# Kernel optimization log

Measured on AMD Instinct MI355X. Metric: run time of the kernel, lower is better.

Reference implementation:

```python
import jax, jax.numpy as jnp
import numpy as np

B, S, DIM, H, HD, K, DEPTH = 2, 2048, 1024, 16, 64, 64, 8
SCALE = 1.0 / np.sqrt(HD)


def _build_cantor_routes(seq_len: int, k: int, depth: int) -> np.ndarray:
    # Vectorized version of CantorAttention._build_cantor_routes
    pos = np.arange(seq_len, dtype=np.float64)
    x = pos / max(1, seq_len - 1)
    x = np.clip(x, 1e-06, 1.0 - 1e-06)
    cantor = np.zeros(seq_len, dtype=np.float64)
    factor = 0.5
    for _ in range(depth):
        x = x * 3.0
        digit = np.floor(x)
        x = x - digit
        cantor += factor * (digit == 2.0)
        factor *= 0.5
    cantor = cantor.astype(np.float32)
    # k nearest positions in Cantor space for each position
    dist = np.abs(cantor[:, None] - cantor[None, :])  # [S, S]
    routes = np.argsort(dist, axis=1, kind='stable')[:, :k]  # [S, k]
    return routes.astype(np.int32)


def setup_inputs() -> dict:
    key = jax.random.key(0)
    k1, k2, k3, k4, k5 = jax.random.split(key, 5)
    s = 1.0 / np.sqrt(DIM)
    return {
        'x': jax.random.normal(k1, (B, S, DIM), dtype=jnp.float32),
        'w_qkv': jax.random.normal(k2, (3 * DIM, DIM), dtype=jnp.float32) * s,
        'b_qkv': jax.random.normal(k3, (3 * DIM,), dtype=jnp.float32) * 0.01,
        'w_out': jax.random.normal(k4, (DIM, DIM), dtype=jnp.float32) * s,
        'b_out': jax.random.normal(k5, (DIM,), dtype=jnp.float32) * 0.01,
        'routes': jnp.asarray(_build_cantor_routes(S, K, DEPTH)),
    }


def reference(x, w_qkv, b_qkv, w_out, b_out, routes):
    b, s, _ = x.shape
    # QKV projection (torch Linear: y = x @ W.T + b)
    qkv = x @ w_qkv.T + b_qkv                       # [B, S, 3*DIM]
    qkv = qkv.reshape(b, s, 3, H, HD).transpose(2, 0, 3, 1, 4)  # [3, B, H, S, HD]
    q, k, v = qkv[0], qkv[1], qkv[2]                # each [B, H, S, HD]
    # Gather k/v at Cantor neighbor routes: [B, H, S, K, HD]
    k_g = jnp.take(k, routes, axis=2)
    v_g = jnp.take(v, routes, axis=2)
    scores = jnp.einsum('bhqd,bhqkd->bhqk', q, k_g) * SCALE
    attn = jax.nn.softmax(scores, axis=-1)
    out = jnp.einsum('bhqk,bhqkd->bhqd', attn, v_g)  # [B, H, S, HD]
    out = out.transpose(0, 2, 1, 3).reshape(b, s, DIM)
    return out @ w_out.T + b_out
```

## Files before the change

kernel.cpp:

```cpp
#include <hip/hip_runtime.h>

#define BQ   2
#define SQ   2048
#define DIMQ 1024
#define HQ   16
#define HDQ  64
#define KQ   64
#define QKV_STRIDE (3 * DIMQ)

typedef __attribute__((ext_vector_type(8))) short short8;
typedef __attribute__((ext_vector_type(4))) float floatx4;

typedef const __attribute__((address_space(1))) unsigned short* gas_t;
typedef __attribute__((address_space(3))) unsigned short* las_t;

__device__ __forceinline__ unsigned short f2b(float f) {
    union { float f; unsigned int u; } x; x.f = f;
    unsigned int r = x.u + 0x7fffu + ((x.u >> 16) & 1u);
    return (unsigned short)(r >> 16);
}
__device__ __forceinline__ float b2f(unsigned short u) {
    union { unsigned int u; float f; } x; x.u = ((unsigned int)u) << 16;
    return x.f;
}

__global__ __launch_bounds__(256) void cast3_f32_bf16(const float* __restrict__ s0, unsigned short* __restrict__ d0, int n0,
                                                      const float* __restrict__ s1, unsigned short* __restrict__ d1, int n1,
                                                      const float* __restrict__ s2, unsigned short* __restrict__ d2, int n2) {
    int i = blockIdx.x * blockDim.x + threadIdx.x;
    const float* s; unsigned short* d;
    if (i < n0)                { s = s0; d = d0; }
    else if (i < n0 + n1)      { s = s1; d = d1; i -= n0; }
    else if (i < n0 + n1 + n2) { s = s2; d = d2; i -= n0 + n1; }
    else return;
    float4 v = ((const float4*)s)[i];
    ushort4 o;
    o.x = f2b(v.x); o.y = f2b(v.y); o.z = f2b(v.z); o.w = f2b(v.w);
    ((ushort4*)d)[i] = o;
}

template <int BM, int BN, typename CT>
__global__ __launch_bounds__(256) void gemm_bf16_nt(const unsigned short* __restrict__ A,
                                                    const unsigned short* __restrict__ B,
                                                    const float* __restrict__ bias,
                                                    CT* __restrict__ C,
                                                    int M, int N, int K) {
    constexpr int MI = BM / 32;
    constexpr int NJ = BN / 32;
    __shared__ unsigned short As[BM * 64];
    __shared__ unsigned short Bs[BN * 64];

    const int tid  = threadIdx.x;
    const int lane = tid & 63;
    const int wv   = tid >> 6;
    const int wm   = (wv >> 1) * (BM / 2);
    const int wn   = (wv & 1) * (BN / 2);
    const int fr   = lane & 15;
    const int fq   = lane >> 4;

    const int m0 = blockIdx.y * BM;
    const int n0 = blockIdx.x * BN;

    floatx4 acc[MI][NJ];
#pragma unroll
    for (int i = 0; i < MI; ++i)
#pragma unroll
        for (int j = 0; j < NJ; ++j) acc[i][j] = (floatx4)(0.f);

    const unsigned short* Ab = A + (size_t)m0 * K;
    const unsigned short* Bb = B + (size_t)n0 * K;

    for (int k0 = 0; k0 < K; k0 += 64) {
#pragma unroll
        for (int c = 0; c < (BM + BN) * 8; c += 256) {
            const int cc = c + tid;
            if (cc < BM * 8) {
                const int row = cc >> 3;
                const int kc  = ((cc & 7) ^ (row & 7)) << 3;
                __builtin_amdgcn_global_load_lds(
                    (gas_t)(Ab + (size_t)row * K + k0 + kc),
                    (las_t)&As[cc * 8], 16, 0, 0);
            } else {
                const int c2  = cc - BM * 8;
                const int row = c2 >> 3;
                const int kc  = ((c2 & 7) ^ (row & 7)) << 3;
                __builtin_amdgcn_global_load_lds(
                    (gas_t)(Bb + (size_t)row * K + k0 + kc),
                    (las_t)&Bs[c2 * 8], 16, 0, 0);
            }
        }
        __syncthreads();

#pragma unroll
        for (int ks = 0; ks < 2; ++ks) {
            short8 af[MI], bf[NJ];
#pragma unroll
            for (int i = 0; i < MI; ++i) {
                const int row = wm + i * 16 + fr;
                const int pos = (ks * 4 + fq) ^ (row & 7);
                af[i] = *(const short8*)&As[row * 64 + pos * 8];
            }
#pragma unroll
            for (int j = 0; j < NJ; ++j) {
                const int row = wn + j * 16 + fr;
                const int pos = (ks * 4 + fq) ^ (row & 7);
                bf[j] = *(const short8*)&Bs[row * 64 + pos * 8];
            }
#pragma unroll
            for (int i = 0; i < MI; ++i)
#pragma unroll
                for (int j = 0; j < NJ; ++j)
                    acc[i][j] = __builtin_amdgcn_mfma_f32_16x16x32_bf16(af[i], bf[j], acc[i][j], 0, 0, 0);
        }
        __syncthreads();
    }

    float bv[NJ];
#pragma unroll
    for (int j = 0; j < NJ; ++j) bv[j] = bias[n0 + wn + j * 16 + fr];
#pragma unroll
    for (int i = 0; i < MI; ++i) {
#pragma unroll
        for (int r = 0; r < 4; ++r) {
            const size_t row = (size_t)(m0 + wm + i * 16 + fq * 4 + r);
#pragma unroll
            for (int j = 0; j < NJ; ++j) {
                const float v = acc[i][j][r] + bv[j];
                if constexpr (sizeof(CT) == 2)
                    C[row * N + n0 + wn + j * 16 + fr] = (CT)f2b(v);
                else
                    C[row * N + n0 + wn + j * 16 + fr] = (CT)v;
            }
        }
    }
}

__global__ __launch_bounds__(256) void attn_kernel(const unsigned short* __restrict__ qkv,
                                                   const int* __restrict__ routes,
                                                   unsigned short* __restrict__ out) {
    __shared__ int   r_s[KQ];
    __shared__ float m_s[128], l_s[128];
    __shared__ float o_part[8][128];

    const int t  = threadIdx.x;
    const int id = blockIdx.x;
    const int bq = (id & 7) * 512 + (id >> 3);
    const int b  = bq >> 11;
    const int q  = bq & 2047;

    if (t < KQ) r_s[t] = routes[q * KQ + t];

    const int g  = t >> 7;
    const int th = t & 127;
    const int h  = th >> 3;
    const int d0 = (t & 7) * 8;

    float qf[8];
    {
        const short8 q8 = *(const short8*)&qkv[((size_t)bq * 3) * DIMQ + h * HDQ + d0];
#pragma unroll
        for (int e = 0; e < 8; ++e) qf[e] = b2f((unsigned short)q8[e]);
    }
    __syncthreads();

    const unsigned short* baseK = qkv + ((size_t)b * SQ * 3 + 1) * DIMQ + h * HDQ + d0;
    const unsigned short* baseV = qkv + ((size_t)b * SQ * 3 + 2) * DIMQ + h * HDQ + d0;

    float m = -1e30f, l = 0.f;
    float o[8];
#pragma unroll
    for (int e = 0; e < 8; ++e) o[e] = 0.f;

    short8 kb[2], vb[2];
#pragma unroll
    for (int i = 0; i < 2; ++i) {
        const size_t roff = (size_t)r_s[i * 2 + g] * QKV_STRIDE;
        kb[i] = *(const short8*)(baseK + roff);
        vb[i] = *(const short8*)(baseV + roff);
    }

#pragma unroll 8
    for (int jj = 0; jj < KQ / 2; ++jj) {
        const int slot = jj & 1;
        const short8 k8 = kb[slot];
        const short8 v8 = vb[slot];
        if (jj + 2 < KQ / 2) {
            const size_t roff = (size_t)r_s[(jj + 2) * 2 + g] * QKV_STRIDE;
            kb[slot] = *(const short8*)(baseK + roff);
            vb[slot] = *(const short8*)(baseV + roff);
        }
        float p = 0.f;
#pragma unroll
        for (int e = 0; e < 8; ++e) p += qf[e] * b2f((unsigned short)k8[e]);
        p += __shfl_xor(p, 1, 64);
        p += __shfl_xor(p, 2, 64);
        p += __shfl_xor(p, 4, 64);
        const float s  = p * 0.125f;
        const float mn = fmaxf(m, s);
        const float al = __expf(m - mn);
        const float pe = __expf(s - mn);
        l = l * al + pe;
#pragma unroll
        for (int e = 0; e < 8; ++e) o[e] = o[e] * al + pe * b2f((unsigned short)v8[e]);
        m = mn;
    }

    if (g == 1) {
        m_s[th] = m; l_s[th] = l;
#pragma unroll
        for (int e = 0; e < 8; ++e) o_part[e][th] = o[e];
    }
    __syncthreads();
    if (g == 0) {
        const float m1 = m_s[th], l1 = l_s[th];
        const float mm = fmaxf(m, m1);
        const float a0 = __expf(m - mm);
        const float a1 = __expf(m1 - mm);
        const float inv = 1.0f / (l * a0 + l1 * a1);
        float oo[8];
#pragma unroll
        for (int e = 0; e < 8; ++e) oo[e] = (o[e] * a0 + o_part[e][th] * a1) * inv;
        ushort4 lo, hi;
        lo.x = f2b(oo[0]); lo.y = f2b(oo[1]); lo.z = f2b(oo[2]); lo.w = f2b(oo[3]);
        hi.x = f2b(oo[4]); hi.y = f2b(oo[5]); hi.z = f2b(oo[6]); hi.w = f2b(oo[7]);
        ushort4* dst = (ushort4*)&out[(size_t)bq * DIMQ + h * HDQ + d0];
        dst[0] = lo; dst[1] = hi;
    }
}

extern "C" void kernel_launch(void* const* d_in, const int* in_sizes, int n_in,
                              void* d_out, int out_size, void* d_ws, size_t ws_size,
                              hipStream_t stream) {
    const float* x      = (const float*)d_in[0];
    const float* w_qkv  = (const float*)d_in[1];
    const float* b_qkv  = (const float*)d_in[2];
    const float* w_out  = (const float*)d_in[3];
    const float* b_out  = (const float*)d_in[4];
    const int*   routes = (const int*)d_in[5];
    float* out = (float*)d_out;

    char* ws = (char*)d_ws;
    unsigned short* qkvb  = (unsigned short*)ws;
    unsigned short* xb    = (unsigned short*)(ws + 25165824);
    unsigned short* attnb = xb;
    unsigned short* wqb   = (unsigned short*)(ws + 33554432);
    unsigned short* wob   = (unsigned short*)(ws + 39845888);

    const int M = BQ * SQ;
    dim3 blk(256);

    {
        const int n0 = M * DIMQ / 4, n1 = 3 * DIMQ * DIMQ / 4, n2 = DIMQ * DIMQ / 4;
        cast3_f32_bf16<<<(n0 + n1 + n2 + 255) / 256, blk, 0, stream>>>(
            x, xb, n0, w_qkv, wqb, n1, w_out, wob, n2);
    }

    gemm_bf16_nt<128, 128, unsigned short><<<dim3(3 * DIMQ / 128, M / 128), blk, 0, stream>>>(
        xb, wqb, b_qkv, qkvb, M, 3 * DIMQ, DIMQ);

    attn_kernel<<<BQ * SQ, blk, 0, stream>>>(qkvb, routes, attnb);

    gemm_bf16_nt<128, 64, float><<<dim3(DIMQ / 64, M / 128), blk, 0, stream>>>(
        attnb, wob, b_out, out, M, DIMQ, DIMQ);
}
```

Measured before the change: 188.0 us.

## Replace online softmax with two-pass exact softmax and base-2 exponent

The gathered attention kernel now computes all 32 scores per thread first, takes one max, exponentiates with exp2f using a query pre-scaled by scale*log2(e), and then accumulates V in a separate loop. This drops the per-step rescaling of the running output and the two exponentials per key that the online softmax needed. The K and V prefetch depth grows from two to four gathered rows. In exchange it holds 32 score registers plus deeper prefetch buffers, which raises register pressure and may lower occupancy, and V loads no longer overlap with the K loop.

```diff
diff --git a/kernel.cpp b/kernel.cpp
--- a/kernel.cpp
+++ b/kernel.cpp
@@ -159,35 +159,27 @@
     {
         const short8 q8 = *(const short8*)&qkv[((size_t)bq * 3) * DIMQ + h * HDQ + d0];
 #pragma unroll
-        for (int e = 0; e < 8; ++e) qf[e] = b2f((unsigned short)q8[e]);
+        for (int e = 0; e < 8; ++e) qf[e] = b2f((unsigned short)q8[e]) * 0.18033688011112042f;
     }
     __syncthreads();
 
     const unsigned short* baseK = qkv + ((size_t)b * SQ * 3 + 1) * DIMQ + h * HDQ + d0;
     const unsigned short* baseV = qkv + ((size_t)b * SQ * 3 + 2) * DIMQ + h * HDQ + d0;
 
-    float m = -1e30f, l = 0.f;
-    float o[8];
-#pragma unroll
-    for (int e = 0; e < 8; ++e) o[e] = 0.f;
-
-    short8 kb[2], vb[2];
-#pragma unroll
-    for (int i = 0; i < 2; ++i) {
+    float s[32];
+    short8 kb[4];
+#pragma unroll
+    for (int i = 0; i < 4; ++i) {
         const size_t roff = (size_t)r_s[i * 2 + g] * QKV_STRIDE;
         kb[i] = *(const short8*)(baseK + roff);
-        vb[i] = *(const short8*)(baseV + roff);
-    }
-
-#pragma unroll 8
-    for (int jj = 0; jj < KQ / 2; ++jj) {
-        const int slot = jj & 1;
+    }
+#pragma unroll
+    for (int jj = 0; jj < 32; ++jj) {
+        const int slot = jj & 3;
         const short8 k8 = kb[slot];
-        const short8 v8 = vb[slot];
-        if (jj + 2 < KQ / 2) {
-            const size_t roff = (size_t)r_s[(jj + 2) * 2 + g] * QKV_STRIDE;
+        if (jj + 4 < 32) {
+            const size_t roff = (size_t)r_s[(jj + 4) * 2 + g] * QKV_STRIDE;
             kb[slot] = *(const short8*)(baseK + roff);
-            vb[slot] = *(const short8*)(baseV + roff);
         }
         float p = 0.f;
 #pragma unroll
@@ -195,14 +187,49 @@
         p += __shfl_xor(p, 1, 64);
         p += __shfl_xor(p, 2, 64);
         p += __shfl_xor(p, 4, 64);
-        const float s  = p * 0.125f;
-        const float mn = fmaxf(m, s);
-        const float al = __expf(m - mn);
-        const float pe = __expf(s - mn);
-        l = l * al + pe;
-#pragma unroll
-        for (int e = 0; e < 8; ++e) o[e] = o[e] * al + pe * b2f((unsigned short)v8[e]);
-        m = mn;
+        s[jj] = p;
+    }
+
+    short8 vb[4];
+#pragma unroll
+    for (int i = 0; i < 4; ++i) {
+        const size_t roff = (size_t)r_s[i * 2 + g] * QKV_STRIDE;
+        vb[i] = *(const short8*)(baseV + roff);
+    }
+
+    float mx[16];
+#pragma unroll
+    for (int i = 0; i < 16; ++i) mx[i] = fmaxf(s[i], s[i + 16]);
+#pragma unroll
+    for (int i = 0; i < 8; ++i) mx[i] = fmaxf(mx[i], mx[i + 8]);
+#pragma unroll
+    for (int i = 0; i < 4; ++i) mx[i] = fmaxf(mx[i], mx[i + 4]);
+    const float m = fmaxf(fmaxf(mx[0], mx[1]), fmaxf(mx[2], mx[3]));
+
+    float l0 = 0.f, l1 = 0.f, l2 = 0.f, l3 = 0.f;
+#pragma unroll
+    for (int jj = 0; jj < 32; jj += 4) {
+        s[jj + 0] = exp2f(s[jj + 0] - m); l0 += s[jj + 0];
+        s[jj + 1] = exp2f(s[jj + 1] - m); l1 += s[jj + 1];
+        s[jj + 2] = exp2f(s[jj + 2] - m); l2 += s[jj + 2];
+        s[jj + 3] = exp2f(s[jj + 3] - m); l3 += s[jj + 3];
+    }
+    const float l = (l0 + l1) + (l2 + l3);
+
+    float o[8];
+#pragma unroll
+    for (int e = 0; e < 8; ++e) o[e] = 0.f;
+#pragma unroll
+    for (int jj = 0; jj < 32; ++jj) {
+        const int slot = jj & 3;
+        const short8 v8 = vb[slot];
+        if (jj + 4 < 32) {
+            const size_t roff = (size_t)r_s[(jj + 4) * 2 + g] * QKV_STRIDE;
+            vb[slot] = *(const short8*)(baseV + roff);
+        }
+        const float p = s[jj];
+#pragma unroll
+        for (int e = 0; e < 8; ++e) o[e] += p * b2f((unsigned short)v8[e]);
     }
 
     if (g == 1) {
@@ -212,11 +239,11 @@
     }
     __syncthreads();
     if (g == 0) {
-        const float m1 = m_s[th], l1 = l_s[th];
+        const float m1 = m_s[th], l1m = l_s[th];
         const float mm = fmaxf(m, m1);
-        const float a0 = __expf(m - mm);
-        const float a1 = __expf(m1 - mm);
-        const float inv = 1.0f / (l * a0 + l1 * a1);
+        const float a0 = exp2f(m - mm);
+        const float a1 = exp2f(m1 - mm);
+        const float inv = 1.0f / (l * a0 + l1m * a1);
         float oo[8];
 #pragma unroll
         for (int e = 0; e < 8; ++e) oo[e] = (o[e] * a0 + o_part[e][th] * a1) * inv;
```

Result: no change. 187.5 us (-0.3%).
